# Kernel optimization log

Hardware: AMD Instinct MI355X
Metric: run time of the kernel (lower is better)

Reference implementation:

```python
import jax, jax.numpy as jnp
import numpy as np

NEG_INF = -1e30  # used via -inf literal below; softmax handles -inf fine


def setup_inputs() -> dict:
    key = jax.random.key(0)
    ks = jax.random.split(key, 5)
    B, S, D, O, E = 8, 2048, 1024, 1024, 8
    scale = 1.0 / np.sqrt(D)
    return {
        "x": jax.random.normal(ks[0], (B, S, D), dtype=jnp.float32),
        "gate_w": jax.random.normal(ks[1], (E, D), dtype=jnp.float32) * scale,
        "gate_b": jnp.zeros((E,), dtype=jnp.float32),
        "expert_w": jax.random.normal(ks[2], (E, O, D), dtype=jnp.float32) * scale,
        "expert_b": jnp.zeros((E, O), dtype=jnp.float32),
    }


K = 2  # top-k from module init


def reference(x, gate_w, gate_b, expert_w, expert_b):
    # Gating on sequence-pooled features: [B, D] -> [B, E]
    pooled = x.mean(axis=1)
    logits = pooled @ gate_w.T + gate_b
    topk_vals, _ = jax.lax.top_k(logits, K)
    min_topk = topk_vals[:, -1:]  # k-th largest per row
    masked = jnp.where(logits < min_topk, -jnp.inf, logits)
    gates = jax.nn.softmax(masked, axis=-1)  # [B, E]

    # All experts computed densely: [B, E, S, O]
    expert_out = jax.nn.gelu(
        jnp.einsum('bsd,eod->beso', x, expert_w) + expert_b[None, :, None, :],
        approximate=False,  # torch GELU default is exact erf form
    )
    # Combine with gating weights: [B, S, O]
    return jnp.einsum('be,beso->bso', gates, expert_out)
```

## Files before the change

kernel.cpp:

```cpp
#include <hip/hip_runtime.h>
#include <stdint.h>

constexpr int Bb = 8;
constexpr int Ss = 2048;
constexpr int Dd = 1024;
constexpr int Oo = 1024;
constexpr int Ee = 8;

typedef __bf16 bf16x8 __attribute__((ext_vector_type(8)));
typedef float  f32x4  __attribute__((ext_vector_type(4)));

__device__ __forceinline__ unsigned short f2bf(float f) {
  unsigned int u = __float_as_uint(f);
  unsigned int r = (u + 0x7fffu + ((u >> 16) & 1u)) >> 16;
  return (unsigned short)r;
}

__device__ __forceinline__ void gl_lds16(const void* g, void* l) {
  __builtin_amdgcn_global_load_lds((const __attribute__((address_space(1))) void*)g,
                                   (__attribute__((address_space(3))) void*)l,
                                   16, 0, 0);
}

__global__ __launch_bounds__(256) void k_prep(
    const float* __restrict__ x, unsigned short* __restrict__ xb,
    const float* __restrict__ w, unsigned short* __restrict__ wb,
    float* __restrict__ pooled) {
  const int bid = blockIdx.x;
  const int t = threadIdx.x;

  if (bid >= 512) {
    const size_t base = (size_t)(bid - 512) * 32768 + t * 4;
    const float4* wp = (const float4*)(w + base);
    ushort4* wo = (ushort4*)(wb + base);
#pragma unroll 8
    for (int it = 0; it < 32; ++it) {
      float4 v = wp[(size_t)it * 256];
      ushort4 o;
      o.x = f2bf(v.x); o.y = f2bf(v.y); o.z = f2bf(v.z); o.w = f2bf(v.w);
      wo[(size_t)it * 256] = o;
    }
    return;
  }

  const int b  = bid >> 6;
  const int sc = bid & 63;
  const size_t base = (size_t)b * Ss * Dd + (size_t)sc * 32 * Dd + t * 4;
  const float4* xp = (const float4*)(x + base);
  ushort4* xo = (ushort4*)(xb + base);
  float4 acc = make_float4(0.f, 0.f, 0.f, 0.f);
#pragma unroll 8
  for (int s = 0; s < 32; ++s) {
    float4 v = xp[(size_t)s * (Dd / 4)];
    acc.x += v.x; acc.y += v.y; acc.z += v.z; acc.w += v.w;
    ushort4 o;
    o.x = f2bf(v.x); o.y = f2bf(v.y); o.z = f2bf(v.z); o.w = f2bf(v.w);
    xo[(size_t)s * (Dd / 4)] = o;
  }
  float* pd = pooled + b * Dd + t * 4;
  atomicAdd(pd + 0, acc.x);
  atomicAdd(pd + 1, acc.y);
  atomicAdd(pd + 2, acc.z);
  atomicAdd(pd + 3, acc.w);
}

__global__ __launch_bounds__(256) void k_gates(
    const float* __restrict__ pooled, const float* __restrict__ gw,
    const float* __restrict__ gb, int* __restrict__ eidx,
    float* __restrict__ egate) {
  __shared__ float slog[Bb * Ee];
  const int t = threadIdx.x;
  const int p = t >> 2, part = t & 3;
  const int b = p >> 3, e = p & 7;
  const float4* pv = (const float4*)(pooled + b * Dd + part * 256);
  const float4* wv = (const float4*)(gw + e * Dd + part * 256);
  float s = 0.f;
#pragma unroll
  for (int i = 0; i < 64; ++i) {
    float4 a = pv[i], w = wv[i];
    s += a.x * w.x + a.y * w.y + a.z * w.z + a.w * w.w;
  }
  s += __shfl_xor(s, 1);
  s += __shfl_xor(s, 2);
  if (part == 0) slog[p] = s * (1.0f / (float)Ss) + gb[e];
  __syncthreads();
  if (t < Bb) {
    float m1 = -3.4e38f, m2 = -3.4e38f;
    int i1 = 0, i2 = 0;
#pragma unroll
    for (int i = 0; i < Ee; ++i) {
      const float v = slog[t * Ee + i];
      if (v > m1) { m2 = m1; i2 = i1; m1 = v; i1 = i; }
      else if (v > m2) { m2 = v; i2 = i; }
    }
    const float e2 = expf(m2 - m1);
    const float inv = 1.0f / (1.0f + e2);
    eidx[t * 2 + 0] = i1;
    eidx[t * 2 + 1] = i2;
    egate[t * 2 + 0] = inv;
    egate[t * 2 + 1] = e2 * inv;
  }
}

constexpr int BM = 128, BN = 64, BK = 64;
constexpr int STG = 32768;
constexpr int OFF_B0 = 16384, OFF_B1 = 24576;

__global__ __launch_bounds__(256, 2) void k_moe_gemm(
    const unsigned short* __restrict__ xb, const unsigned short* __restrict__ wb,
    const int* __restrict__ eidx, const float* __restrict__ egate,
    const float* __restrict__ expert_b, float* __restrict__ out) {
  __shared__ char lds[2 * STG];

  const int hw = blockIdx.x;
  const int lg_id = ((hw & 7) << 8) | (hw >> 3);
  const int b  = lg_id >> 8;
  const int m0 = (lg_id & 15) * BM;
  const int n0 = ((lg_id >> 4) & 15) * BN;
  const int t  = threadIdx.x;
  const int lane = t & 63;
  const int wid  = t >> 6;
  const int wr = wid >> 1, wc = wid & 1;
  const int lr = lane & 15;
  const int lg = lane >> 4;

  const int e0 = eidx[b * 2 + 0];
  const int e1 = eidx[b * 2 + 1];
  const float g0 = egate[b * 2 + 0];
  const float g1 = egate[b * 2 + 1];

  const int srow = t >> 3;
  const int scol = (((t & 7) ^ (srow & 7)) * 8);
  const int ldsoff = wid * 1024;

  const unsigned short* Abase  = xb + (size_t)b * Ss * Dd + (size_t)m0 * Dd;
  const unsigned short* B0base = wb + (size_t)e0 * Oo * Dd + (size_t)n0 * Dd;
  const unsigned short* B1base = wb + (size_t)e1 * Oo * Dd + (size_t)n0 * Dd;

  f32x4 acc0[4][2] = {};
  f32x4 acc1[4][2] = {};

  auto STAGE = [&](int st, int kt) {
    char* base = lds + st * STG;
#pragma unroll
    for (int h = 0; h < 4; ++h) {
      const int row = srow + h * 32;
      gl_lds16(Abase + (size_t)row * Dd + kt + scol,
               base + h * 4096 + ldsoff);
    }
#pragma unroll
    for (int h = 0; h < 2; ++h) {
      const int row = srow + h * 32;
      const size_t goff = (size_t)row * Dd + kt + scol;
      gl_lds16(B0base + goff, base + OFF_B0 + h * 4096 + ldsoff);
      gl_lds16(B1base + goff, base + OFF_B1 + h * 4096 + ldsoff);
    }
  };

  auto COMPUTE = [&](int st) {
    const char* base = lds + st * STG;
#pragma unroll
    for (int ks = 0; ks < 2; ++ks) {
      const int ul = (ks << 2) | lg;
      bf16x8 af[4], bf0[2], bf1[2];
#pragma unroll
      for (int m = 0; m < 4; ++m) {
        const int r = wr * 64 + m * 16 + lr;
        af[m] = *(const bf16x8*)(base + r * 128 + ((ul ^ (r & 7)) << 4));
      }
#pragma unroll
      for (int n = 0; n < 2; ++n) {
        const int r = wc * 32 + n * 16 + lr;
        bf0[n] = *(const bf16x8*)(base + OFF_B0 + r * 128 + ((ul ^ (r & 7)) << 4));
        bf1[n] = *(const bf16x8*)(base + OFF_B1 + r * 128 + ((ul ^ (r & 7)) << 4));
      }
#pragma unroll
      for (int m = 0; m < 4; ++m)
#pragma unroll
        for (int n = 0; n < 2; ++n) {
          acc0[m][n] = __builtin_amdgcn_mfma_f32_16x16x32_bf16(
              af[m], bf0[n], acc0[m][n], 0, 0, 0);
          acc1[m][n] = __builtin_amdgcn_mfma_f32_16x16x32_bf16(
              af[m], bf1[n], acc1[m][n], 0, 0, 0);
        }
    }
  };

  STAGE(0, 0);
  int cur = 0;
#pragma unroll 1
  for (int kt_i = 0; kt_i < 15; ++kt_i) {
    STAGE(cur ^ 1, (kt_i + 1) * BK);
    asm volatile("s_waitcnt vmcnt(8)" ::: "memory");
    __builtin_amdgcn_s_barrier();
    __builtin_amdgcn_sched_barrier(0);
    COMPUTE(cur);
    __builtin_amdgcn_s_barrier();
    __builtin_amdgcn_sched_barrier(0);
    cur ^= 1;
  }
  asm volatile("s_waitcnt vmcnt(0)" ::: "memory");
  __builtin_amdgcn_s_barrier();
  __builtin_amdgcn_sched_barrier(0);
  COMPUTE(cur);

#pragma unroll
  for (int n = 0; n < 2; ++n) {
    const int col = n0 + wc * 32 + n * 16 + lr;
    const float bias0 = expert_b[e0 * Oo + col];
    const float bias1 = expert_b[e1 * Oo + col];
#pragma unroll
    for (int m = 0; m < 4; ++m)
#pragma unroll
      for (int r = 0; r < 4; ++r) {
        const int row = m0 + wr * 64 + m * 16 + lg * 4 + r;
        const float v0 = acc0[m][n][r] + bias0;
        const float v1 = acc1[m][n][r] + bias1;
        const float ge0 = 0.5f * v0 * (1.0f + erff(v0 * 0.70710678118654752f));
        const float ge1 = 0.5f * v1 * (1.0f + erff(v1 * 0.70710678118654752f));
        out[(size_t)b * Ss * Oo + (size_t)row * Oo + col] = g0 * ge0 + g1 * ge1;
      }
  }
}

extern "C" void kernel_launch(void* const* d_in, const int* in_sizes, int n_in,
                              void* d_out, int out_size, void* d_ws, size_t ws_size,
                              hipStream_t stream) {
  const float* x        = (const float*)d_in[0];
  const float* gate_w   = (const float*)d_in[1];
  const float* gate_b   = (const float*)d_in[2];
  const float* expert_w = (const float*)d_in[3];
  const float* expert_b = (const float*)d_in[4];
  float* out = (float*)d_out;

  char* ws = (char*)d_ws;
  float* pooled = (float*)ws;
  int*   eidx   = (int*)(ws + 32832);
  float* egate  = (float*)(ws + 32896);
  unsigned short* xb = (unsigned short*)(ws + 65536);
  unsigned short* wb = (unsigned short*)(ws + 65536 + (size_t)Bb * Ss * Dd * 2);

  hipMemsetAsync(pooled, 0, Bb * Dd * sizeof(float), stream);

  k_prep<<<768, 256, 0, stream>>>(x, xb, expert_w, wb, pooled);
  k_gates<<<1, 256, 0, stream>>>(pooled, gate_w, gate_b, eidx, egate);
  k_moe_gemm<<<(Ss / BM) * (Oo / BN) * Bb, 256, 0, stream>>>(xb, wb, eidx, egate,
                                                             expert_b, out);
}
```

Measured before the change: 280.1 us.

## Enlarge MoE GEMM tiles to 256x128 with 8 waves and split-phase MFMA schedule

Grows the block tile from 128x64 to 256x128 with BK=32, runs 512 threads (8 waves), and rewrites the K loop as a macro-unrolled double-buffered pipeline. Each k-step now does two MFMA phases, one per expert weight, with barriers, s_setprio and a new swizzle for 64-byte rows. The larger tile raises arithmetic intensity and data reuse per LDS load, which should cut global and LDS traffic. In exchange it uses more accumulator registers (32 f32x4 per thread), launches far fewer blocks (512 for the grid), and adds extra barriers per k-step.

```diff
diff --git a/kernel.cpp b/kernel.cpp
--- a/kernel.cpp
+++ b/kernel.cpp
@@ -102,25 +102,27 @@
   }
 }
 
-constexpr int BM = 128, BN = 64, BK = 64;
+constexpr int BM = 256, BN = 128, BK = 32;
 constexpr int STG = 32768;
-constexpr int OFF_B0 = 16384, OFF_B1 = 24576;
-
-__global__ __launch_bounds__(256, 2) void k_moe_gemm(
+constexpr int B0_OFF = 16384, B1_OFF = 24576;
+
+__global__ __launch_bounds__(512, 2) void k_moe_gemm(
     const unsigned short* __restrict__ xb, const unsigned short* __restrict__ wb,
     const int* __restrict__ eidx, const float* __restrict__ egate,
     const float* __restrict__ expert_b, float* __restrict__ out) {
   __shared__ char lds[2 * STG];
 
   const int hw = blockIdx.x;
-  const int lg_id = ((hw & 7) << 8) | (hw >> 3);
-  const int b  = lg_id >> 8;
-  const int m0 = (lg_id & 15) * BM;
-  const int n0 = ((lg_id >> 4) & 15) * BN;
+  const int lg_id = ((hw & 7) << 6) | (hw >> 3);
+  const int b  = lg_id >> 6;
+  const int wg = lg_id & 63;
+  const int m0 = (wg & 7) * BM;
+  const int n0 = (wg >> 3) * BN;
   const int t  = threadIdx.x;
   const int lane = t & 63;
   const int wid  = t >> 6;
-  const int wr = wid >> 1, wc = wid & 1;
+  const int wr = wid >> 2;
+  const int wc = wid & 3;
   const int lr = lane & 15;
   const int lg = lane >> 4;
 
@@ -129,80 +131,83 @@
   const float g0 = egate[b * 2 + 0];
   const float g1 = egate[b * 2 + 1];
 
-  const int srow = t >> 3;
-  const int scol = (((t & 7) ^ (srow & 7)) * 8);
+  const int srow = t >> 2;
+  const int scol = ((t & 3) ^ ((srow >> 1) & 3)) * 8;
   const int ldsoff = wid * 1024;
 
-  const unsigned short* Abase  = xb + (size_t)b * Ss * Dd + (size_t)m0 * Dd;
-  const unsigned short* B0base = wb + (size_t)e0 * Oo * Dd + (size_t)n0 * Dd;
-  const unsigned short* B1base = wb + (size_t)e1 * Oo * Dd + (size_t)n0 * Dd;
-
-  f32x4 acc0[4][2] = {};
-  f32x4 acc1[4][2] = {};
-
-  auto STAGE = [&](int st, int kt) {
-    char* base = lds + st * STG;
-#pragma unroll
-    for (int h = 0; h < 4; ++h) {
-      const int row = srow + h * 32;
-      gl_lds16(Abase + (size_t)row * Dd + kt + scol,
-               base + h * 4096 + ldsoff);
-    }
-#pragma unroll
-    for (int h = 0; h < 2; ++h) {
-      const int row = srow + h * 32;
-      const size_t goff = (size_t)row * Dd + kt + scol;
-      gl_lds16(B0base + goff, base + OFF_B0 + h * 4096 + ldsoff);
-      gl_lds16(B1base + goff, base + OFF_B1 + h * 4096 + ldsoff);
-    }
+  const unsigned short* gA0 = xb + (size_t)b * Ss * Dd + (size_t)(m0 + srow) * Dd + scol;
+  const unsigned short* gA1 = gA0 + (size_t)128 * Dd;
+  const unsigned short* gB0 = wb + (size_t)e0 * Oo * Dd + (size_t)(n0 + srow) * Dd + scol;
+  const unsigned short* gB1 = wb + (size_t)e1 * Oo * Dd + (size_t)(n0 + srow) * Dd + scol;
+
+  const int swz = (lg ^ ((lr >> 1) & 3)) * 16;
+  const int adsA0 = (wr * 128 + lr) * 64 + swz;
+  const int adsA1 = adsA0 + STG;
+  const int adsB0 = B0_OFF + (wc * 32 + lr) * 64 + swz;
+  const int adsB1 = adsB0 + STG;
+
+  f32x4 acc0[8][2] = {};
+  f32x4 acc1[8][2] = {};
+
+  auto STAGE = [&](char* base) {
+    gl_lds16(gA0, base + ldsoff);
+    gl_lds16(gA1, base + 8192 + ldsoff);
+    gl_lds16(gB0, base + B0_OFF + ldsoff);
+    gl_lds16(gB1, base + B1_OFF + ldsoff);
+    gA0 += BK; gA1 += BK; gB0 += BK; gB1 += BK;
   };
 
-  auto COMPUTE = [&](int st) {
-    const char* base = lds + st * STG;
-#pragma unroll
-    for (int ks = 0; ks < 2; ++ks) {
-      const int ul = (ks << 2) | lg;
-      bf16x8 af[4], bf0[2], bf1[2];
-#pragma unroll
-      for (int m = 0; m < 4; ++m) {
-        const int r = wr * 64 + m * 16 + lr;
-        af[m] = *(const bf16x8*)(base + r * 128 + ((ul ^ (r & 7)) << 4));
-      }
-#pragma unroll
-      for (int n = 0; n < 2; ++n) {
-        const int r = wc * 32 + n * 16 + lr;
-        bf0[n] = *(const bf16x8*)(base + OFF_B0 + r * 128 + ((ul ^ (r & 7)) << 4));
-        bf1[n] = *(const bf16x8*)(base + OFF_B1 + r * 128 + ((ul ^ (r & 7)) << 4));
-      }
-#pragma unroll
-      for (int m = 0; m < 4; ++m)
-#pragma unroll
-        for (int n = 0; n < 2; ++n) {
-          acc0[m][n] = __builtin_amdgcn_mfma_f32_16x16x32_bf16(
-              af[m], bf0[n], acc0[m][n], 0, 0, 0);
-          acc1[m][n] = __builtin_amdgcn_mfma_f32_16x16x32_bf16(
-              af[m], bf1[n], acc1[m][n], 0, 0, 0);
-        }
-    }
-  };
-
-  STAGE(0, 0);
-  int cur = 0;
+#define TILE(ADSA, ADSB, STAGEBASE, DOSTAGE, VMC)                              \
+  {                                                                            \
+    if (DOSTAGE) STAGE(STAGEBASE);                                             \
+    asm volatile("s_waitcnt vmcnt(" VMC ")" ::: "memory");                     \
+    __builtin_amdgcn_s_barrier();                                              \
+    __builtin_amdgcn_sched_barrier(0);                                         \
+    bf16x8 af[8], bf[2];                                                       \
+    _Pragma("unroll")                                                          \
+    for (int m = 0; m < 8; ++m)                                                \
+      af[m] = *(const bf16x8*)(lds + (ADSA) + m * 1024);                       \
+    _Pragma("unroll")                                                          \
+    for (int n = 0; n < 2; ++n)                                                \
+      bf[n] = *(const bf16x8*)(lds + (ADSB) + n * 1024);                       \
+    __builtin_amdgcn_s_barrier();                                              \
+    asm volatile("s_waitcnt lgkmcnt(0)" ::: "memory");                         \
+    __builtin_amdgcn_sched_barrier(0);                                         \
+    __builtin_amdgcn_s_setprio(1);                                             \
+    _Pragma("unroll")                                                          \
+    for (int m = 0; m < 8; ++m)                                                \
+      _Pragma("unroll")                                                        \
+      for (int n = 0; n < 2; ++n)                                              \
+        acc0[m][n] = __builtin_amdgcn_mfma_f32_16x16x32_bf16(                  \
+            af[m], bf[n], acc0[m][n], 0, 0, 0);                                \
+    __builtin_amdgcn_s_setprio(0);                                             \
+    __builtin_amdgcn_s_barrier();                                              \
+    _Pragma("unroll")                                                          \
+    for (int n = 0; n < 2; ++n)                                                \
+      bf[n] = *(const bf16x8*)(lds + (ADSB) + 8192 + n * 1024);                \
+    asm volatile("s_waitcnt lgkmcnt(0)" ::: "memory");                         \
+    __builtin_amdgcn_sched_barrier(0);                                         \
+    __builtin_amdgcn_s_setprio(1);                                             \
+    _Pragma("unroll")                                                          \
+    for (int m = 0; m < 8; ++m)                                                \
+      _Pragma("unroll")                                                        \
+      for (int n = 0; n < 2; ++n)                                              \
+        acc1[m][n] = __builtin_amdgcn_mfma_f32_16x16x32_bf16(                  \
+            af[m], bf[n], acc1[m][n], 0, 0, 0);                                \
+    __builtin_amdgcn_s_setprio(0);                                             \
+    __builtin_amdgcn_s_barrier();                                              \
+  }
+
+  STAGE(lds);
 #pragma unroll 1
-  for (int kt_i = 0; kt_i < 15; ++kt_i) {
-    STAGE(cur ^ 1, (kt_i + 1) * BK);
-    asm volatile("s_waitcnt vmcnt(8)" ::: "memory");
-    __builtin_amdgcn_s_barrier();
-    __builtin_amdgcn_sched_barrier(0);
-    COMPUTE(cur);
-    __builtin_amdgcn_s_barrier();
-    __builtin_amdgcn_sched_barrier(0);
-    cur ^= 1;
-  }
-  asm volatile("s_waitcnt vmcnt(0)" ::: "memory");
-  __builtin_amdgcn_s_barrier();
-  __builtin_amdgcn_sched_barrier(0);
-  COMPUTE(cur);
+  for (int i = 0; i < 15; ++i) {
+    TILE(adsA0, adsB0, lds + STG, 1, "4");
+    TILE(adsA1, adsB1, lds,       1, "4");
+  }
+  TILE(adsA0, adsB0, lds + STG, 1, "4");
+  TILE(adsA1, adsB1, lds,       0, "0");
+
+#undef TILE
 
 #pragma unroll
   for (int n = 0; n < 2; ++n) {
@@ -210,10 +215,10 @@
     const float bias0 = expert_b[e0 * Oo + col];
     const float bias1 = expert_b[e1 * Oo + col];
 #pragma unroll
-    for (int m = 0; m < 4; ++m)
+    for (int m = 0; m < 8; ++m)
 #pragma unroll
       for (int r = 0; r < 4; ++r) {
-        const int row = m0 + wr * 64 + m * 16 + lg * 4 + r;
+        const int row = m0 + wr * 128 + m * 16 + lg * 4 + r;
         const float v0 = acc0[m][n][r] + bias0;
         const float v1 = acc1[m][n][r] + bias1;
         const float ge0 = 0.5f * v0 * (1.0f + erff(v0 * 0.70710678118654752f));
@@ -244,6 +249,6 @@
 
   k_prep<<<768, 256, 0, stream>>>(x, xb, expert_w, wb, pooled);
   k_gates<<<1, 256, 0, stream>>>(pooled, gate_w, gate_b, eidx, egate);
-  k_moe_gemm<<<(Ss / BM) * (Oo / BN) * Bb, 256, 0, stream>>>(xb, wb, eidx, egate,
+  k_moe_gemm<<<(Ss / BM) * (Oo / BN) * Bb, 512, 0, stream>>>(xb, wb, eidx, egate,
                                                              expert_b, out);
 }
```

Measured after the change: 275.8 us. Within noise of the previous version (-1.5%).
